# Kernel tuning notes

Hardware: AMD Instinct MI355X
Metric: run time of the kernel (lower is better)

## Reference

```python
import jax, jax.numpy as jnp
import numpy as np

B, S, HID, QK, H = 2, 2048, 2048, 2048, 16
DK, DV = QK // H, HID // H
EPS = 1e-5


def setup_inputs() -> dict:
    key = jax.random.key(0)
    ks = jax.random.split(key, 8)
    sd = 1.0 / np.sqrt(HID)
    inp = {
        "x": jax.random.normal(ks[0], (B, S, HID), jnp.float32),
        "wq": jax.random.normal(ks[1], (HID, QK), jnp.float32) * sd,
        "bq": jnp.zeros((QK,), jnp.float32),
        "wk": jax.random.normal(ks[2], (HID, QK), jnp.float32) * sd,
        "bk": jnp.zeros((QK,), jnp.float32),
        "wv": jax.random.normal(ks[3], (HID, HID), jnp.float32) * sd,
        "bv": jnp.zeros((HID,), jnp.float32),
        "wg": jax.random.normal(ks[4], (HID, HID), jnp.float32) * sd,
        "bg": jnp.zeros((HID,), jnp.float32),
        "wo": jax.random.normal(ks[5], (HID, HID), jnp.float32) * sd,
        "bo": jnp.zeros((HID,), jnp.float32),
        "gn_w": jnp.ones((HID,), jnp.float32),
        "gn_b": jnp.zeros((HID,), jnp.float32),
        # RetNet default gammas: 1 - exp(linspace(log(1/32), log(1/512), H))
        "gamma": 1.0 - jnp.exp(jnp.linspace(-np.log(32.0), -np.log(512.0), H)).astype(jnp.float32),
    }
    return inp


def reference(x, wq, bq, wk, bk, wv, bv, wg, bg, wo, bo, gn_w, gn_b, gamma):
    b, s, hid = x.shape
    h = gamma.shape[0]
    dk = wq.shape[1] // h
    dv = hid // h
    # projections + head split -> (b, h, s, d)
    q = (x @ wq + bq).reshape(b, s, h, dk).transpose(0, 2, 1, 3)
    k = (x @ wk + bk).reshape(b, s, h, dk).transpose(0, 2, 1, 3)
    v = (x @ wv + bv).reshape(b, s, h, dv).transpose(0, 2, 1, 3)
    # causal decay mask: gamma^(n-m) for n >= m else 0  -> (h, s, s)
    idx = jnp.arange(s)
    diff = idx[:, None] - idx[None, :]
    expn = jnp.maximum(diff, 0).astype(x.dtype)
    dmask = jnp.where(diff >= 0, gamma[:, None, None] ** expn, 0.0)
    # parallel retention
    scores = jnp.einsum('bhnd,bhmd->bhnm', q, k) * dmask
    ret = jnp.einsum('bhnm,bhmv->bhnv', scores, v)  # (b, h, s, dv)
    # GroupNorm(num_groups=h) over (b, hid, s): stats per (b, head) over (s, dv)
    mean = ret.mean(axis=(2, 3), keepdims=True)
    var = ((ret - mean) ** 2).mean(axis=(2, 3), keepdims=True)
    norm = (ret - mean) * jax.lax.rsqrt(var + EPS)
    norm = norm * gn_w.reshape(h, dv)[None, :, None, :] + gn_b.reshape(h, dv)[None, :, None, :]
    ro = norm.transpose(0, 2, 1, 3).reshape(b, s, hid)  # (b, s, hid)
    gate = jax.nn.silu(x @ wg + bg)
    out = (gate * ro) @ wo + bo
    return out
```

## Files before the change

### kernel.cpp

```cpp
#include <hip/hip_runtime.h>
#include <cstdint>
#include <cstddef>

#define DEVI __device__ __forceinline__

typedef unsigned short u16;
typedef __bf16 bf16_t;
typedef bf16_t bf16x8 __attribute__((ext_vector_type(8)));
typedef float f32x4 __attribute__((ext_vector_type(4)));

constexpr int BB = 2, SS = 2048, HID = 2048, NH = 16, DK = 128, DV = 128;
constexpr int MR = BB * SS;
constexpr int KD = HID;

DEVI u16 f2bf(float f) {
  union { float f; uint32_t u; } v; v.f = f;
  uint32_t u = v.u;
  uint32_t r = u + 0x7FFFu + ((u >> 16) & 1u);
  return (u16)(r >> 16);
}
DEVI float bf2f(u16 h) {
  union { uint32_t u; float f; } v; v.u = ((uint32_t)h) << 16;
  return v.f;
}
DEVI f32x4 mfma16(bf16x8 a, bf16x8 b, f32x4 c) {
  return __builtin_amdgcn_mfma_f32_16x16x32_bf16(a, b, c, 0, 0, 0);
}

__global__ __launch_bounds__(256) void wtrans_kernel(
    const float* __restrict__ wq, const float* __restrict__ wk,
    const float* __restrict__ wv, const float* __restrict__ wg,
    const float* __restrict__ wo, u16* __restrict__ wt)
{
  __shared__ float t[32][33];
  const float* srcs[5] = {wq, wk, wv, wg, wo};
  const float* W = srcs[blockIdx.z];
  u16* dst = wt + (size_t)blockIdx.z * (size_t)KD * HID;
  int tx = threadIdx.x, ty = threadIdx.y;
  int c0 = blockIdx.x * 32, r0 = blockIdx.y * 32;
#pragma unroll
  for (int i = 0; i < 4; ++i)
    t[ty + i * 8][tx] = W[(size_t)(r0 + ty + i * 8) * HID + c0 + tx];
  __syncthreads();
#pragma unroll
  for (int i = 0; i < 4; ++i) {
    int n = c0 + ty + i * 8;
    int k = r0 + tx;
    dst[(size_t)n * KD + k] = f2bf(t[tx][ty + i * 8]);
  }
}

template<bool AF32>
DEVI void gemm_core(const void* __restrict__ Ap, const u16* __restrict__ Bt,
                    int m0, int n0, u16* sA, u16* sB, f32x4 (&acc)[4][4])
{
  const int tid = threadIdx.x;
  const int lane = tid & 63;
  const int wave = tid >> 6;
  const int wr = wave >> 1, wc = wave & 1;
  const int lhi = lane >> 4, llo = lane & 15;

  for (int kt = 0; kt < KD / 64; ++kt) {
    __syncthreads();
    if (AF32) {
      const float* A = (const float*)Ap;
#pragma unroll
      for (int i = 0; i < 8; ++i) {
        int c = tid + i * 256;
        int row = c >> 4, col4 = c & 15;
        float4 v = *(const float4*)(A + (size_t)(m0 + row) * KD + kt * 64 + col4 * 4);
        ushort4 hh;
        hh.x = f2bf(v.x); hh.y = f2bf(v.y); hh.z = f2bf(v.z); hh.w = f2bf(v.w);
        *(ushort4*)((char*)sA + row * 128 + ((col4 * 8) ^ ((row & 7) << 4))) = hh;
      }
    } else {
      const u16* A = (const u16*)Ap;
#pragma unroll
      for (int i = 0; i < 4; ++i) {
        int c = tid + i * 256;
        int row = c >> 3, col8 = c & 7;
        uint4 v = *(const uint4*)(A + (size_t)(m0 + row) * KD + kt * 64 + col8 * 8);
        *(uint4*)((char*)sA + row * 128 + ((col8 * 16) ^ ((row & 7) << 4))) = v;
      }
    }
#pragma unroll
    for (int i = 0; i < 4; ++i) {
      int c = tid + i * 256;
      int row = c >> 3, col8 = c & 7;
      uint4 v = *(const uint4*)(Bt + (size_t)(n0 + row) * KD + kt * 64 + col8 * 8);
      *(uint4*)((char*)sB + row * 128 + ((col8 * 16) ^ ((row & 7) << 4))) = v;
    }
    __syncthreads();
#pragma unroll
    for (int ks = 0; ks < 2; ++ks) {
      const int kb = ks * 64 + lhi * 16;
      bf16x8 af[4], bfr[4];
#pragma unroll
      for (int mi = 0; mi < 4; ++mi) {
        int row = wr * 64 + mi * 16 + llo;
        af[mi] = *(const bf16x8*)((char*)sA + row * 128 + (kb ^ ((row & 7) << 4)));
      }
#pragma unroll
      for (int ni = 0; ni < 4; ++ni) {
        int row = wc * 64 + ni * 16 + llo;
        bfr[ni] = *(const bf16x8*)((char*)sB + row * 128 + (kb ^ ((row & 7) << 4)));
      }
#pragma unroll
      for (int mi = 0; mi < 4; ++mi)
#pragma unroll
        for (int ni = 0; ni < 4; ++ni)
          acc[mi][ni] = mfma16(af[mi], bfr[ni], acc[mi][ni]);
    }
  }
}

__global__ __launch_bounds__(256) void proj_kernel(
    const float* __restrict__ x, const u16* __restrict__ wtBase,
    const float* __restrict__ bq, const float* __restrict__ bk,
    const float* __restrict__ bv, const float* __restrict__ bg,
    u16* __restrict__ qb, u16* __restrict__ kb,
    u16* __restrict__ vtb, u16* __restrict__ gb)
{
  __shared__ u16 sA[128 * 64];
  __shared__ u16 sB[128 * 64];
  const int z = blockIdx.z;
  const u16* Bt = wtBase + (size_t)z * (size_t)KD * HID;
  f32x4 acc[4][4];
  const f32x4 zero = {0.f, 0.f, 0.f, 0.f};
#pragma unroll
  for (int mi = 0; mi < 4; ++mi)
#pragma unroll
    for (int ni = 0; ni < 4; ++ni) acc[mi][ni] = zero;

  const int m0 = blockIdx.x * 128, n0 = blockIdx.y * 128;
  gemm_core<true>(x, Bt, m0, n0, sA, sB, acc);

  const float* bias = (z == 0) ? bq : (z == 1) ? bk : (z == 2) ? bv : bg;
  const int lane = threadIdx.x & 63, wave = threadIdx.x >> 6;
  const int wr = wave >> 1, wc = wave & 1;
  const int lhi = lane >> 4, llo = lane & 15;
#pragma unroll
  for (int mi = 0; mi < 4; ++mi) {
#pragma unroll
    for (int ni = 0; ni < 4; ++ni) {
      int row0 = m0 + wr * 64 + mi * 16 + lhi * 4;
      int n = n0 + wc * 64 + ni * 16 + llo;
      float bsn = bias[n];
      if (z == 2) {
        int b = row0 >> 11, s0 = row0 & (SS - 1);
        int h = n >> 7, j = n & 127;
        ushort4 hv;
        hv.x = f2bf(acc[mi][ni][0] + bsn);
        hv.y = f2bf(acc[mi][ni][1] + bsn);
        hv.z = f2bf(acc[mi][ni][2] + bsn);
        hv.w = f2bf(acc[mi][ni][3] + bsn);
        *(ushort4*)(vtb + ((size_t)((b * NH + h) * DV + j)) * SS + s0) = hv;
      } else if (z == 3) {
#pragma unroll
        for (int r = 0; r < 4; ++r) {
          int m = row0 + r;
          float c = acc[mi][ni][r] + bsn;
          float sg = c / (1.0f + expf(-c));
          gb[(size_t)m * HID + n] = f2bf(sg);
        }
      } else {
        u16* dst = (z == 0) ? qb : kb;
#pragma unroll
        for (int r = 0; r < 4; ++r) {
          int m = row0 + r;
          int b = m >> 11, s = m & (SS - 1);
          int h = n >> 7, j = n & 127;
          dst[((size_t)((b * NH + h) * SS + s)) * DK + j] = f2bf(acc[mi][ni][r] + bsn);
        }
      }
    }
  }
}

__global__ __launch_bounds__(256) void retention_kernel(
    const u16* __restrict__ qb, const u16* __restrict__ kb,
    const u16* __restrict__ vtb, const float* __restrict__ gamma,
    float* __restrict__ ret, float* __restrict__ stats)
{
  __shared__ u16 sK[64 * 128];
  __shared__ u16 sV[128 * 64];
  __shared__ u16 sP[4][32 * 64];
  __shared__ float red[8];

  const int bh = blockIdx.y;
  const int n0 = blockIdx.x * 128;
  const int h = bh & (NH - 1);
  const float lg2 = log2f(gamma[h]);

  const int tid = threadIdx.x, lane = tid & 63, wave = tid >> 6;
  const int lhi = lane >> 4, llo = lane & 15;
  const int qrow = n0 + wave * 32;

  const u16* qbase = qb + ((size_t)bh * SS + qrow) * DK;
  bf16x8 aq[2][4];
#pragma unroll
  for (int mi = 0; mi < 2; ++mi)
#pragma unroll
    for (int ks = 0; ks < 4; ++ks)
      aq[mi][ks] = *(const bf16x8*)(qbase + (size_t)(mi * 16 + llo) * DK + ks * 32 + lhi * 8);

  float rdec[2][4];
#pragma unroll
  for (int mi = 0; mi < 2; ++mi)
#pragma unroll
    for (int r = 0; r < 4; ++r)
      rdec[mi][r] = exp2f(lg2 * (float)(qrow + mi * 16 + lhi * 4 + r));

  const f32x4 zero = {0.f, 0.f, 0.f, 0.f};
  f32x4 oacc[2][8];
#pragma unroll
  for (int mi = 0; mi < 2; ++mi)
#pragma unroll
    for (int nj = 0; nj < 8; ++nj) oacc[mi][nj] = zero;

  const u16* kbase = kb + (size_t)bh * SS * DK;
  const u16* vbase = vtb + (size_t)bh * DV * SS;
  const int mtiles = n0 / 64 + 2;

  for (int mt = 0; mt < mtiles; ++mt) {
    const int m0 = mt * 64;
    __syncthreads();
#pragma unroll
    for (int i = 0; i < 4; ++i) {
      int c = tid + i * 256;
      int row = c >> 4, col8 = c & 15;
      uint4 v = *(const uint4*)(kbase + (size_t)(m0 + row) * DK + col8 * 8);
      *(uint4*)((char*)sK + row * 256 + ((col8 * 16) ^ ((row & 15) << 4))) = v;
    }
#pragma unroll
    for (int i = 0; i < 4; ++i) {
      int c = tid + i * 256;
      int row = c >> 3, col8 = c & 7;
      uint4 v = *(const uint4*)(vbase + (size_t)row * SS + m0 + col8 * 8);
      *(uint4*)((char*)sV + row * 128 + ((col8 * 16) ^ ((row & 7) << 4))) = v;
    }
    __syncthreads();

    f32x4 sacc[2][4];
#pragma unroll
    for (int mi = 0; mi < 2; ++mi)
#pragma unroll
      for (int ni = 0; ni < 4; ++ni) sacc[mi][ni] = zero;
#pragma unroll
    for (int ks = 0; ks < 4; ++ks) {
      const int kbyte = ks * 64 + lhi * 16;
      bf16x8 bk_[4];
#pragma unroll
      for (int ni = 0; ni < 4; ++ni) {
        int row = ni * 16 + llo;
        bk_[ni] = *(const bf16x8*)((char*)sK + row * 256 + (kbyte ^ ((row & 15) << 4)));
      }
#pragma unroll
      for (int mi = 0; mi < 2; ++mi)
#pragma unroll
        for (int ni = 0; ni < 4; ++ni)
          sacc[mi][ni] = mfma16(aq[mi][ks], bk_[ni], sacc[mi][ni]);
    }

    float cfac[4];
#pragma unroll
    for (int ni = 0; ni < 4; ++ni)
      cfac[ni] = exp2f(-lg2 * (float)(m0 + ni * 16 + llo));
    const bool masked = (m0 + 63 > qrow);
    char* myP = (char*)&sP[wave][0];
#pragma unroll
    for (int mi = 0; mi < 2; ++mi) {
#pragma unroll
      for (int ni = 0; ni < 4; ++ni) {
#pragma unroll
        for (int r = 0; r < 4; ++r) {
          int prow = mi * 16 + lhi * 4 + r;
          int pcol = ni * 16 + llo;
          float w = rdec[mi][r] * cfac[ni];
          if (masked && (qrow + prow < m0 + pcol)) w = 0.0f;
          float p = sacc[mi][ni][r] * w;
          *(u16*)(myP + prow * 128 + ((pcol * 2) ^ ((prow & 7) << 4))) = f2bf(p);
        }
      }
    }

#pragma unroll
    for (int ks2 = 0; ks2 < 2; ++ks2) {
      const int kbyte = ks2 * 64 + lhi * 16;
      bf16x8 pa[2];
#pragma unroll
      for (int mi = 0; mi < 2; ++mi) {
        int row = mi * 16 + llo;
        pa[mi] = *(const bf16x8*)(myP + row * 128 + (kbyte ^ ((row & 7) << 4)));
      }
#pragma unroll
      for (int nj = 0; nj < 8; ++nj) {
        int row = nj * 16 + llo;
        bf16x8 vb = *(const bf16x8*)((char*)sV + row * 128 + (kbyte ^ ((row & 7) << 4)));
#pragma unroll
        for (int mi = 0; mi < 2; ++mi)
          oacc[mi][nj] = mfma16(pa[mi], vb, oacc[mi][nj]);
      }
    }
  }

  float lsum = 0.f, lsq = 0.f;
  float* rbase = ret + ((size_t)bh * SS + qrow) * DV;
#pragma unroll
  for (int mi = 0; mi < 2; ++mi) {
#pragma unroll
    for (int nj = 0; nj < 8; ++nj) {
      int prow0 = mi * 16 + lhi * 4;
      int j = nj * 16 + llo;
#pragma unroll
      for (int r = 0; r < 4; ++r) {
        float v = oacc[mi][nj][r];
        rbase[(size_t)(prow0 + r) * DV + j] = v;
        lsum += v; lsq += v * v;
      }
    }
  }
#pragma unroll
  for (int off = 32; off > 0; off >>= 1) {
    lsum += __shfl_down(lsum, off, 64);
    lsq  += __shfl_down(lsq,  off, 64);
  }
  if (lane == 0) { red[wave * 2] = lsum; red[wave * 2 + 1] = lsq; }
  __syncthreads();
  if (tid == 0) {
    float s = red[0] + red[2] + red[4] + red[6];
    float q = red[1] + red[3] + red[5] + red[7];
    atomicAdd(&stats[bh * 2], s);
    atomicAdd(&stats[bh * 2 + 1], q);
  }
}

__global__ __launch_bounds__(256) void normgate_kernel(
    const float* __restrict__ ret, const u16* __restrict__ gb,
    const float* __restrict__ stats, const float* __restrict__ gn_w,
    const float* __restrict__ gn_b, u16* __restrict__ a2)
{
  const int idx4 = (blockIdx.x * 256 + threadIdx.x) * 4;
  const int bh = idx4 >> 18;
  const int rem = idx4 & (SS * DV - 1);
  const int s = rem >> 7;
  const int dv = rem & (DV - 1);
  const float inv = 1.0f / (float)(SS * DV);
  float mean = stats[bh * 2] * inv;
  float var = stats[bh * 2 + 1] * inv - mean * mean;
  float rstd = rsqrtf(var + 1e-5f);
  const int b = bh >> 4, h = bh & (NH - 1);
  const int hd = h * DV + dv;
  float4 rv = *(const float4*)(ret + idx4);
  float4 w4 = *(const float4*)(gn_w + hd);
  float4 b4 = *(const float4*)(gn_b + hd);
  size_t gidx = ((size_t)(b * SS + s)) * HID + hd;
  ushort4 g4 = *(const ushort4*)(gb + gidx);
  ushort4 o;
  o.x = f2bf(bf2f(g4.x) * ((rv.x - mean) * rstd * w4.x + b4.x));
  o.y = f2bf(bf2f(g4.y) * ((rv.y - mean) * rstd * w4.y + b4.y));
  o.z = f2bf(bf2f(g4.z) * ((rv.z - mean) * rstd * w4.z + b4.z));
  o.w = f2bf(bf2f(g4.w) * ((rv.w - mean) * rstd * w4.w + b4.w));
  *(ushort4*)(a2 + gidx) = o;
}

__global__ __launch_bounds__(256) void final_kernel(
    const u16* __restrict__ a2, const u16* __restrict__ woT,
    const float* __restrict__ bo, float* __restrict__ out)
{
  __shared__ u16 sA[128 * 64];
  __shared__ u16 sB[128 * 64];
  f32x4 acc[4][4];
  const f32x4 zero = {0.f, 0.f, 0.f, 0.f};
#pragma unroll
  for (int mi = 0; mi < 4; ++mi)
#pragma unroll
    for (int ni = 0; ni < 4; ++ni) acc[mi][ni] = zero;

  const int m0 = blockIdx.x * 128, n0 = blockIdx.y * 128;
  gemm_core<false>(a2, woT, m0, n0, sA, sB, acc);

  const int lane = threadIdx.x & 63, wave = threadIdx.x >> 6;
  const int wr = wave >> 1, wc = wave & 1;
  const int lhi = lane >> 4, llo = lane & 15;
#pragma unroll
  for (int mi = 0; mi < 4; ++mi) {
#pragma unroll
    for (int ni = 0; ni < 4; ++ni) {
      int row0 = m0 + wr * 64 + mi * 16 + lhi * 4;
      int n = n0 + wc * 64 + ni * 16 + llo;
      float bn = bo[n];
#pragma unroll
      for (int r = 0; r < 4; ++r)
        out[(size_t)(row0 + r) * HID + n] = acc[mi][ni][r] + bn;
    }
  }
}

extern "C" void kernel_launch(void* const* d_in, const int* in_sizes, int n_in,
                              void* d_out, int out_size, void* d_ws, size_t ws_size,
                              hipStream_t stream) {
  const float* x    = (const float*)d_in[0];
  const float* wq   = (const float*)d_in[1];
  const float* bq   = (const float*)d_in[2];
  const float* wk   = (const float*)d_in[3];
  const float* bk   = (const float*)d_in[4];
  const float* wv   = (const float*)d_in[5];
  const float* bv   = (const float*)d_in[6];
  const float* wg   = (const float*)d_in[7];
  const float* bg   = (const float*)d_in[8];
  const float* wo   = (const float*)d_in[9];
  const float* bo   = (const float*)d_in[10];
  const float* gn_w = (const float*)d_in[11];
  const float* gn_b = (const float*)d_in[12];
  const float* gam  = (const float*)d_in[13];

  char* ws = (char*)d_ws;
  u16* wT    = (u16*)(ws);
  u16* qb    = (u16*)(ws + 41943040);
  u16* kbuf  = (u16*)(ws + 58720256);
  u16* vtb   = (u16*)(ws + 75497472);
  u16* gb    = (u16*)(ws + 92274688);
  float* ret = (float*)(ws + 109051904);
  float* st  = (float*)(ws + 142606336);
  u16* a2    = qb;

  hipMemsetAsync(st, 0, 256, stream);
  wtrans_kernel<<<dim3(64, 64, 5), dim3(32, 8), 0, stream>>>(wq, wk, wv, wg, wo, wT);
  proj_kernel<<<dim3(32, 16, 4), 256, 0, stream>>>(x, wT, bq, bk, bv, bg, qb, kbuf, vtb, gb);
  retention_kernel<<<dim3(16, 32), 256, 0, stream>>>(qb, kbuf, vtb, gam, ret, st);
  normgate_kernel<<<16384, 256, 0, stream>>>(ret, gb, st, gn_w, gn_b, a2);
  final_kernel<<<dim3(32, 16), 256, 0, stream>>>(a2, wT + (size_t)4 * KD * HID, bo, (float*)d_out);
}
```

Measured before the change: 606.7 us.

## Use direct global-to-LDS loads and pre-cast x to bf16 once

Adds a kernel that casts x to bf16 once, so the projection GEMM no longer reloads and converts fp32 x in every N-tile block. The GEMM and retention tile loads now use global_load_lds (16-byte direct-to-LDS DMA) with the XOR swizzle moved onto the source address, which skips the register round trip. This costs one extra launch and a bf16 copy of x stored in the ret buffer region. The swizzle correctness depends on the per-wave contiguous LDS destination layout.

```diff
diff --git a/kernel.cpp b/kernel.cpp
--- a/kernel.cpp
+++ b/kernel.cpp
@@ -25,6 +25,24 @@
 }
 DEVI f32x4 mfma16(bf16x8 a, bf16x8 b, f32x4 c) {
   return __builtin_amdgcn_mfma_f32_16x16x32_bf16(a, b, c, 0, 0, 0);
+}
+DEVI void gload16(const u16* g, u16* l) {
+  __builtin_amdgcn_global_load_lds(
+      (const __attribute__((address_space(1))) uint32_t*)g,
+      (__attribute__((address_space(3))) uint32_t*)l, 16, 0, 0);
+}
+
+__global__ __launch_bounds__(256) void castx_kernel(
+    const float* __restrict__ x, u16* __restrict__ xb)
+{
+  size_t i = ((size_t)blockIdx.x * 256 + threadIdx.x) * 8;
+  float4 a = *(const float4*)(x + i);
+  float4 b = *(const float4*)(x + i + 4);
+  ushort4 lo, hi;
+  lo.x = f2bf(a.x); lo.y = f2bf(a.y); lo.z = f2bf(a.z); lo.w = f2bf(a.w);
+  hi.x = f2bf(b.x); hi.y = f2bf(b.y); hi.z = f2bf(b.z); hi.w = f2bf(b.w);
+  *(ushort4*)(xb + i) = lo;
+  *(ushort4*)(xb + i + 4) = hi;
 }
 
 __global__ __launch_bounds__(256) void wtrans_kernel(
@@ -50,8 +68,7 @@
   }
 }
 
-template<bool AF32>
-DEVI void gemm_core(const void* __restrict__ Ap, const u16* __restrict__ Bt,
+DEVI void gemm_core(const u16* __restrict__ A, const u16* __restrict__ Bt,
                     int m0, int n0, u16* sA, u16* sB, f32x4 (&acc)[4][4])
 {
   const int tid = threadIdx.x;
@@ -62,33 +79,21 @@
 
   for (int kt = 0; kt < KD / 64; ++kt) {
     __syncthreads();
-    if (AF32) {
-      const float* A = (const float*)Ap;
-#pragma unroll
-      for (int i = 0; i < 8; ++i) {
-        int c = tid + i * 256;
-        int row = c >> 4, col4 = c & 15;
-        float4 v = *(const float4*)(A + (size_t)(m0 + row) * KD + kt * 64 + col4 * 4);
-        ushort4 hh;
-        hh.x = f2bf(v.x); hh.y = f2bf(v.y); hh.z = f2bf(v.z); hh.w = f2bf(v.w);
-        *(ushort4*)((char*)sA + row * 128 + ((col4 * 8) ^ ((row & 7) << 4))) = hh;
-      }
-    } else {
-      const u16* A = (const u16*)Ap;
-#pragma unroll
-      for (int i = 0; i < 4; ++i) {
-        int c = tid + i * 256;
-        int row = c >> 3, col8 = c & 7;
-        uint4 v = *(const uint4*)(A + (size_t)(m0 + row) * KD + kt * 64 + col8 * 8);
-        *(uint4*)((char*)sA + row * 128 + ((col8 * 16) ^ ((row & 7) << 4))) = v;
-      }
-    }
 #pragma unroll
     for (int i = 0; i < 4; ++i) {
-      int c = tid + i * 256;
-      int row = c >> 3, col8 = c & 7;
-      uint4 v = *(const uint4*)(Bt + (size_t)(n0 + row) * KD + kt * 64 + col8 * 8);
-      *(uint4*)((char*)sB + row * 128 + ((col8 * 16) ^ ((row & 7) << 4))) = v;
+      int c = i * 256 + wave * 64 + lane;
+      int row = c >> 3, scol = c & 7;
+      int dcol = scol ^ (row & 7);
+      gload16(A + (size_t)(m0 + row) * KD + kt * 64 + dcol * 8,
+              sA + (i * 256 + wave * 64) * 8);
+    }
+#pragma unroll
+    for (int i = 0; i < 4; ++i) {
+      int c = i * 256 + wave * 64 + lane;
+      int row = c >> 3, scol = c & 7;
+      int dcol = scol ^ (row & 7);
+      gload16(Bt + (size_t)(n0 + row) * KD + kt * 64 + dcol * 8,
+              sB + (i * 256 + wave * 64) * 8);
     }
     __syncthreads();
 #pragma unroll
@@ -115,7 +120,7 @@
 }
 
 __global__ __launch_bounds__(256) void proj_kernel(
-    const float* __restrict__ x, const u16* __restrict__ wtBase,
+    const u16* __restrict__ xb, const u16* __restrict__ wtBase,
     const float* __restrict__ bq, const float* __restrict__ bk,
     const float* __restrict__ bv, const float* __restrict__ bg,
     u16* __restrict__ qb, u16* __restrict__ kb,
@@ -133,7 +138,7 @@
     for (int ni = 0; ni < 4; ++ni) acc[mi][ni] = zero;
 
   const int m0 = blockIdx.x * 128, n0 = blockIdx.y * 128;
-  gemm_core<true>(x, Bt, m0, n0, sA, sB, acc);
+  gemm_core(xb, Bt, m0, n0, sA, sB, acc);
 
   const float* bias = (z == 0) ? bq : (z == 1) ? bk : (z == 2) ? bv : bg;
   const int lane = threadIdx.x & 63, wave = threadIdx.x >> 6;
@@ -227,17 +232,19 @@
     __syncthreads();
 #pragma unroll
     for (int i = 0; i < 4; ++i) {
-      int c = tid + i * 256;
-      int row = c >> 4, col8 = c & 15;
-      uint4 v = *(const uint4*)(kbase + (size_t)(m0 + row) * DK + col8 * 8);
-      *(uint4*)((char*)sK + row * 256 + ((col8 * 16) ^ ((row & 15) << 4))) = v;
+      int c = i * 256 + wave * 64 + lane;
+      int row = c >> 4, scol = c & 15;
+      int dcol = scol ^ (row & 15);
+      gload16(kbase + (size_t)(m0 + row) * DK + dcol * 8,
+              sK + (i * 256 + wave * 64) * 8);
     }
 #pragma unroll
     for (int i = 0; i < 4; ++i) {
-      int c = tid + i * 256;
-      int row = c >> 3, col8 = c & 7;
-      uint4 v = *(const uint4*)(vbase + (size_t)row * SS + m0 + col8 * 8);
-      *(uint4*)((char*)sV + row * 128 + ((col8 * 16) ^ ((row & 7) << 4))) = v;
+      int c = i * 256 + wave * 64 + lane;
+      int row = c >> 3, scol = c & 7;
+      int dcol = scol ^ (row & 7);
+      gload16(vbase + (size_t)row * SS + m0 + dcol * 8,
+              sV + (i * 256 + wave * 64) * 8);
     }
     __syncthreads();
 
@@ -378,7 +385,7 @@
     for (int ni = 0; ni < 4; ++ni) acc[mi][ni] = zero;
 
   const int m0 = blockIdx.x * 128, n0 = blockIdx.y * 128;
-  gemm_core<false>(a2, woT, m0, n0, sA, sB, acc);
+  gemm_core(a2, woT, m0, n0, sA, sB, acc);
 
   const int lane = threadIdx.x & 63, wave = threadIdx.x >> 6;
   const int wr = wave >> 1, wc = wave & 1;
@@ -424,10 +431,12 @@
   float* ret = (float*)(ws + 109051904);
   float* st  = (float*)(ws + 142606336);
   u16* a2    = qb;
+  u16* xb    = (u16*)ret;
 
   hipMemsetAsync(st, 0, 256, stream);
+  castx_kernel<<<4096, 256, 0, stream>>>(x, xb);
   wtrans_kernel<<<dim3(64, 64, 5), dim3(32, 8), 0, stream>>>(wq, wk, wv, wg, wo, wT);
-  proj_kernel<<<dim3(32, 16, 4), 256, 0, stream>>>(x, wT, bq, bk, bv, bg, qb, kbuf, vtb, gb);
+  proj_kernel<<<dim3(32, 16, 4), 256, 0, stream>>>(xb, wT, bq, bk, bv, bg, qb, kbuf, vtb, gb);
   retention_kernel<<<dim3(16, 32), 256, 0, stream>>>(qb, kbuf, vtb, gam, ret, st);
   normgate_kernel<<<16384, 256, 0, stream>>>(ret, gb, st, gn_w, gn_b, a2);
   final_kernel<<<dim3(32, 16), 256, 0, stream>>>(a2, wT + (size_t)4 * KD * HID, bo, (float*)d_out);
```

Result: faster. 555.7 us (-8.4%).
